# Kernel tuning notes

Measured on AMD Instinct MI355X. Metric: run time of the kernel, lower is better.

The kernel has to match this reference:

```python
import jax, jax.numpy as jnp
import numpy as np


def setup_inputs() -> dict:
    key = jax.random.key(0)
    kz, kh, k0 = jax.random.split(key, 3)
    B, C, D, H, W = 2, 96, 32, 32, 32
    z = jax.random.uniform(kz, (B, C, D, H, W), dtype=jnp.float32)  # gate in [0,1]
    h_tilde = jax.random.normal(kh, (B, C, D, H, W), dtype=jnp.float32)  # candidate state
    h0 = jax.random.uniform(k0, (1,), dtype=jnp.float32)  # scalar initial state
    return {"z": z, "h_tilde": h_tilde, "h0": h0}


def reference(z, h_tilde, h0):
    """GruDirection3d with d1=d2=d3=1 (forward_3, no flips).

    The three wavefront slice-updates in the torch code jointly implement
        out[d, y, x] = z[d, y, x] * h_tilde[d, y, x]
                       + (1 - z[d, y, x]) * out[d-1, y-1, x-1]
    with out == h0 whenever any index goes below 0 (the padded border).
    We realize it as t_num = min(D, H, W) full-volume shifted updates: after
    iteration k, all voxels with min(d, y, x) <= k-1 hold their final value,
    so after t_num iterations the result matches the torch wavefront DP exactly.
    """
    B, C, D, H, W = z.shape
    t_num = min(D, H, W)  # static shapes -> python int, jit-safe
    # padded state: index 0 along each spatial axis is the h0 border (never written)
    h_pad = jnp.full((B, C, D + 1, H + 1, W + 1), h0[0], dtype=z.dtype)

    one = jnp.asarray(1, dtype=z.dtype)

    def step(h_pad, _):
        prev = h_pad[:, :, :-1, :-1, :-1]  # out[d-1, y-1, x-1] (with border = h0)
        new = z * h_tilde + (one - z) * prev
        return h_pad.at[:, :, 1:, 1:, 1:].set(new), None

    h_pad, _ = jax.lax.scan(step, h_pad, None, length=t_num)
    return h_pad[:, :, 1:, 1:, 1:]
```

## Files before the change

### kernel.cpp

```cpp
#include <hip/hip_runtime.h>
#include <hip/hip_bf16.h>


#define PLANE 1024
#define DD 32

__global__ __launch_bounds__(1024) void gru3d_wavefront(
    const float* __restrict__ z,
    const float* __restrict__ ht,
    const float* __restrict__ h0p,
    float* __restrict__ out)
{
    __shared__ float buf[2][PLANE];

    const int bc  = blockIdx.x;
    const int tid = threadIdx.x;
    const int y   = tid >> 5;
    const int x   = tid & 31;
    const float h0 = h0p[0];

    const float* zb = z   + (size_t)bc * (DD * PLANE);
    const float* tb = ht  + (size_t)bc * (DD * PLANE);
    float*       ob = out + (size_t)bc * (DD * PLANE);

    float zA = zb[tid];
    float tA = tb[tid];
    float zB = zb[PLANE + tid];
    float tB = tb[PLANE + tid];

    float h = zA * tA + (1.0f - zA) * h0;
    ob[tid] = h;
    buf[0][tid] = h;
    __syncthreads();

    const bool interior = (y > 0) & (x > 0);

    #pragma unroll 4
    for (int d = 1; d < DD; ++d) {
        zA = zB; tA = tB;
        if (d + 1 < DD) {
            zB = zb[(d + 1) * PLANE + tid];
            tB = tb[(d + 1) * PLANE + tid];
        }
        float pv = interior ? buf[(d - 1) & 1][tid - 33] : h0;
        float hn = zA * tA + (1.0f - zA) * pv;
        ob[d * PLANE + tid] = hn;
        buf[d & 1][tid] = hn;
        __syncthreads();
    }
}

extern "C" void kernel_launch(void* const* d_in, const int* in_sizes, int n_in,
                              void* d_out, int out_size, void* d_ws, size_t ws_size,
                              hipStream_t stream) {
    const float* z  = (const float*)d_in[0];
    const float* ht = (const float*)d_in[1];
    const float* h0 = (const float*)d_in[2];
    float* out      = (float*)d_out;

    const int BC = 2 * 96;
    gru3d_wavefront<<<dim3(BC), dim3(1024), 0, stream>>>(z, ht, h0, out);
}
```

Baseline: 100.9 us.

## Parallelize recurrence along independent diagonal chains instead of plane wavefront

Each thread now follows one diagonal chain (d,y,x)->(d+1,y+1,x+1) from a boundary voxel, carrying the state in a register. This removes shared memory and the per-plane block barriers, and spreads the work over three times as many blocks. Chain lengths vary widely, which causes load imbalance, and some groups of threads access memory with larger strides. The update is rewritten as h += z*(t-h), which changes rounding slightly.

```diff
diff --git a/kernel.cpp b/kernel.cpp
--- a/kernel.cpp
+++ b/kernel.cpp
@@ -1,52 +1,53 @@
 #include <hip/hip_runtime.h>
-#include <hip/hip_bf16.h>
 
 
-#define PLANE 1024
-#define DD 32
+#define SLAB   32768
+#define STRIDE 1057
 
-__global__ __launch_bounds__(1024) void gru3d_wavefront(
+__global__ __launch_bounds__(1024) void gru3d_diag(
     const float* __restrict__ z,
     const float* __restrict__ ht,
     const float* __restrict__ h0p,
     float* __restrict__ out)
 {
-    __shared__ float buf[2][PLANE];
+    const int tid  = threadIdx.x;
+    const int slab = blockIdx.x / 3;
+    const int i    = (blockIdx.x % 3) * 1024 + tid;
 
-    const int bc  = blockIdx.x;
-    const int tid = threadIdx.x;
-    const int y   = tid >> 5;
-    const int x   = tid & 31;
+    int d0, y0, x0;
+    if (i < 1024) {
+        d0 = 0;
+        y0 = i >> 5;
+        x0 = i & 31;
+    } else if (i < 2016) {
+        const int j = i - 1024;
+        d0 = 1 + (j >> 5);
+        y0 = 0;
+        x0 = j & 31;
+    } else if (i < 2977) {
+        const int j = i - 2016;
+        d0 = 1 + j / 31;
+        y0 = 1 + j % 31;
+        x0 = 0;
+    } else {
+        return;
+    }
+
+    const int len = 32 - max(d0, max(y0, x0));
+
     const float h0 = h0p[0];
+    const size_t base = (size_t)slab * SLAB + (size_t)(d0 * 1024 + y0 * 32 + x0);
+    const float* __restrict__ zp = z   + base;
+    const float* __restrict__ tp = ht  + base;
+    float*       __restrict__ op = out + base;
 
-    const float* zb = z   + (size_t)bc * (DD * PLANE);
-    const float* tb = ht  + (size_t)bc * (DD * PLANE);
-    float*       ob = out + (size_t)bc * (DD * PLANE);
-
-    float zA = zb[tid];
-    float tA = tb[tid];
-    float zB = zb[PLANE + tid];
-    float tB = tb[PLANE + tid];
-
-    float h = zA * tA + (1.0f - zA) * h0;
-    ob[tid] = h;
-    buf[0][tid] = h;
-    __syncthreads();
-
-    const bool interior = (y > 0) & (x > 0);
-
+    float h = h0;
     #pragma unroll 4
-    for (int d = 1; d < DD; ++d) {
-        zA = zB; tA = tB;
-        if (d + 1 < DD) {
-            zB = zb[(d + 1) * PLANE + tid];
-            tB = tb[(d + 1) * PLANE + tid];
-        }
-        float pv = interior ? buf[(d - 1) & 1][tid - 33] : h0;
-        float hn = zA * tA + (1.0f - zA) * pv;
-        ob[d * PLANE + tid] = hn;
-        buf[d & 1][tid] = hn;
-        __syncthreads();
+    for (int k = 0; k < len; ++k) {
+        const float zv = zp[(size_t)k * STRIDE];
+        const float tv = tp[(size_t)k * STRIDE];
+        h += zv * (tv - h);
+        op[(size_t)k * STRIDE] = h;
     }
 }
 
@@ -59,5 +60,5 @@
     float* out      = (float*)d_out;
 
     const int BC = 2 * 96;
-    gru3d_wavefront<<<dim3(BC), dim3(1024), 0, stream>>>(z, ht, h0, out);
+    gru3d_diag<<<dim3(BC * 3), dim3(1024), 0, stream>>>(z, ht, h0, out);
 }
```

Measured after the change: 146.3 us. 45.1% more time.
